# Kernel tuning notes

Hardware: AMD Instinct MI355X
Metric: run time of the kernel (lower is better)

The kernel has to match this reference:

```python
import jax, jax.numpy as jnp
import numpy as np

N = 50000          # nodes
E = 1_600_000      # edges (avg degree 32)
F_IN = 48          # node features (df columns 1:-1)
H, C = 8, 8        # conv1: 8 heads x 8 channels
NC = 2             # num_classes
NEG_SLOPE = 0.2    # PyG GATConv default leaky_relu slope


def setup_inputs() -> dict:
    key = jax.random.key(0)
    ks = jax.random.split(key, 9)
    s = 0.1
    return {
        "x": jax.random.normal(ks[0], (N, F_IN), jnp.float32),
        "edge_index": jax.random.randint(ks[1], (2, E), 0, N, dtype=jnp.int64),
        "W1": jax.random.normal(ks[2], (F_IN, H * C), jnp.float32) * s,
        "att_src1": jax.random.normal(ks[3], (H, C), jnp.float32) * s,
        "att_dst1": jax.random.normal(ks[4], (H, C), jnp.float32) * s,
        "b1": jnp.zeros((H * C,), jnp.float32),
        "W2": jax.random.normal(ks[5], (H * C, NC), jnp.float32) * s,
        "att_src2": jax.random.normal(ks[6], (1, NC), jnp.float32) * s,
        "att_dst2": jax.random.normal(ks[7], (1, NC), jnp.float32) * s,
        "b2": jnp.zeros((NC,), jnp.float32),
    }


def _gat_conv(x, src, dst, W, a_src, a_dst, b, heads, out_ch, concat):
    """PyG GATConv: linear -> per-edge leaky_relu attention -> segment softmax
    over destination nodes -> scatter-sum aggregation."""
    n = x.shape[0]
    h = (x @ W).reshape(n, heads, out_ch)               # [N, H, C]
    e_src = (h * a_src).sum(-1)                          # [N, H]
    e_dst = (h * a_dst).sum(-1)                          # [N, H]
    e = jax.nn.leaky_relu(e_src[src] + e_dst[dst], NEG_SLOPE)  # [E, H]
    # numerically stable segment softmax over incoming edges of each dst node
    m = jax.ops.segment_max(e, dst, num_segments=n)      # [N, H]
    ex = jnp.exp(e - m[dst])
    den = jax.ops.segment_sum(ex, dst, num_segments=n)   # [N, H]
    alpha = ex / den[dst]                                # [E, H]
    out = jax.ops.segment_sum(h[src] * alpha[:, :, None], dst, num_segments=n)
    out = out.reshape(n, heads * out_ch) if concat else out.mean(axis=1)
    return out + b


def reference(x, edge_index, W1, att_src1, att_dst1, b1, W2, att_src2, att_dst2, b2):
    n = x.shape[0]
    loop = jnp.arange(n, dtype=edge_index.dtype)  # GATConv add_self_loops=True
    src = jnp.concatenate([edge_index[0], loop])
    dst = jnp.concatenate([edge_index[1], loop])
    h = _gat_conv(x, src, dst, W1, att_src1, att_dst1, b1, H, C, True)
    h = jax.nn.elu(h)
    out = _gat_conv(h, src, dst, W2, att_src2, att_dst2, b2, 1, NC, False)
    return jax.nn.log_softmax(out, axis=1)
```

## Files before the change

### kernel.cpp

```cpp
#include <hip/hip_runtime.h>
#include <hip/hip_bf16.h>
#include <math.h>

#define NN 50000
#define FIN 48
#define HC 64
#define NHEAD 8
#define NCH 8
#define NCLS 2
#define NEG 0.2f
#define LOG2E 1.44269504f

#define NPB 98
#define NBKT 512
#define CAP 4096
#define BCHUNK 4096


__global__ void k_bin_h1(const int* __restrict__ ei, int* __restrict__ bcur,
                         int* __restrict__ pairs, int e, int tot, int nbin,
                         const float* __restrict__ x, const float* __restrict__ W1,
                         const float* __restrict__ as1, const float* __restrict__ ad1,
                         __hip_bfloat16* __restrict__ h1b, __hip_bfloat16* __restrict__ es1b,
                         float* __restrict__ ed1, int n) {
    __shared__ int hist[NBKT];
    __shared__ int gbase[NBKT];
    __shared__ float Wl[FIN * HC];
    __shared__ float xs[4][FIN];
    __shared__ float hr[4][HC];
    int t = threadIdx.x;
    if ((int)blockIdx.x < nbin) {
        hist[t] = 0; hist[t + 256] = 0;
        __syncthreads();
        int base = blockIdx.x * BCHUNK;
        int end = min(base + BCHUNK, tot);
        int pk[16];
        int bp[16];
        #pragma unroll
        for (int k = 0; k < 16; ++k) {
            int i = base + t + k * 256;
            if (i < end) {
                int s, d;
                if (i < e) { s = ei[i]; d = ei[e + i]; }
                else       { s = d = i - e; }
                int b = d / NPB;
                int p = atomicAdd(&hist[b], 1);
                pk[k] = ((d - b * NPB) << 16) | s;
                bp[k] = (b << 16) | p;
            }
        }
        __syncthreads();
        for (int u = t; u < NBKT; u += 256) {
            int h = hist[u];
            gbase[u] = h ? atomicAdd(&bcur[u], h) : 0;
        }
        __syncthreads();
        #pragma unroll
        for (int k = 0; k < 16; ++k) {
            int i = base + t + k * 256;
            if (i < end) {
                int b = bp[k] >> 16;
                int p = gbase[b] + (bp[k] & 0xFFFF);
                if (p < CAP) pairs[b * CAP + p] = pk[k];
            }
        }
    } else {
        for (int i = t; i < FIN * HC; i += 256) Wl[i] = W1[i];
        int ngroups = (n + 3) >> 2;
        int nl = t >> 6, j = t & 63;
        for (int g = blockIdx.x - nbin; g < ngroups; g += gridDim.x - nbin) {
            int nb = g * 4;
            __syncthreads();
            for (int i = t; i < 4 * FIN; i += 256) {
                int l = i / FIN, k = i % FIN;
                int nd = nb + l;
                xs[l][k] = (nd < n) ? x[nd * FIN + k] : 0.f;
            }
            __syncthreads();
            float acc = 0.f;
            #pragma unroll
            for (int k = 0; k < FIN; ++k) acc += xs[nl][k] * Wl[k * HC + j];
            int nd = nb + nl;
            if (nd < n) h1b[nd * HC + j] = __float2bfloat16(acc);
            hr[nl][j] = acc;
            __syncthreads();
            if (j < 16 && nd < n) {
                int hh = j & 7;
                const float* av = (j < 8) ? as1 : ad1;
                float ev = 0.f;
                #pragma unroll
                for (int c = 0; c < NCH; ++c) ev += hr[nl][hh * NCH + c] * av[hh * NCH + c];
                ev *= LOG2E;
                if (j < 8) es1b[nd * NHEAD + hh] = __float2bfloat16(ev);
                else       ed1[nd * NHEAD + hh] = ev;
            }
        }
    }
}


__global__ void k_bucket_csr(const int* __restrict__ pairs, const int* __restrict__ bcur,
                             int* __restrict__ rowptr, int* __restrict__ degv,
                             int* __restrict__ csr, int n) {
    __shared__ int hist[256];
    int b = blockIdx.x, t = threadIdx.x;
    int lo = b * NPB;
    int nn = min(NPB, n - lo);
    if (nn <= 0) return;
    int base = b * CAP;
    int cnt = min(bcur[b], CAP);
    hist[t] = 0;
    __syncthreads();
    int srcv[16];
    int kp[16];
    #pragma unroll
    for (int k = 0; k < 16; ++k) {
        int i = t + k * 256;
        if (i < cnt) {
            int p = pairs[base + i];
            int key = p >> 16;
            int pos = atomicAdd(&hist[key], 1);
            srcv[k] = p & 0xFFFF;
            kp[k] = (key << 16) | pos;
        }
    }
    __syncthreads();
    int v = hist[t];
    for (int off = 1; off < 256; off <<= 1) {
        int y = (t >= off) ? hist[t - off] : 0;
        __syncthreads();
        hist[t] += y;
        __syncthreads();
    }
    int excl = hist[t] - v;
    if (t < nn) { rowptr[lo + t] = base + excl; degv[lo + t] = v; }
    __syncthreads();
    hist[t] = excl;
    __syncthreads();
    #pragma unroll
    for (int k = 0; k < 16; ++k) {
        int i = t + k * 256;
        if (i < cnt) {
            int key = kp[k] >> 16, pos = kp[k] & 0xFFFF;
            csr[base + hist[key] + pos] = srcv[k];
        }
    }
}


__global__ void k_agg1(const __hip_bfloat16* __restrict__ h1b, const __hip_bfloat16* __restrict__ es1b,
                       const float* __restrict__ ed1, const int* __restrict__ rowptr,
                       const int* __restrict__ degv, const int* __restrict__ csr,
                       const float* __restrict__ b1,
                       const float* __restrict__ W2, const float* __restrict__ as2,
                       const float* __restrict__ ad2, float4* __restrict__ node2, int n) {
    int wid = (blockIdx.x * blockDim.x + threadIdx.x) >> 6;
    if (wid >= n) return;
    int lane = threadIdx.x & 63;
    int j  = lane >> 3;
    int hw = lane & 7;
    int e4 = lane >> 4;
    int r  = lane & 15;
    int ha = r >> 1;
    int ch0 = (ha << 3) + ((r & 1) << 2);
    int wbase = (e4 << 3) + ha;
    int start = rowptr[wid];
    int cnt = degv[wid];
    float edv = ed1[wid * NHEAD + hw];
    float sumw = 0.f;
    float a0 = 0.f, a1 = 0.f, a2 = 0.f, a3 = 0.f;
    int nbatch = cnt >> 3;

    int rv = csr[start + min(lane, cnt - 1)];

    int sl; float ev; uint2 va, vb;
    if (nbatch > 0) {
        sl = __shfl(rv, j, 64);
        ev = __bfloat162float(es1b[sl * NHEAD + hw]);
        int su0 = __shfl(sl, e4 << 3, 64);
        int su1 = __shfl(sl, (4 + e4) << 3, 64);
        va = *(const uint2*)(h1b + su0 * HC + ch0);
        vb = *(const uint2*)(h1b + su1 * HC + ch0);
        for (int b = 1; b < nbatch; ++b) {
            int sl_n;
            if (b < 8) sl_n = __shfl(rv, (b << 3) + j, 64);
            else       sl_n = csr[start + (b << 3) + j];
            float ev_n = __bfloat162float(es1b[sl_n * NHEAD + hw]);
            int su0n = __shfl(sl_n, e4 << 3, 64);
            int su1n = __shfl(sl_n, (4 + e4) << 3, 64);
            uint2 va_n = *(const uint2*)(h1b + su0n * HC + ch0);
            uint2 vb_n = *(const uint2*)(h1b + su1n * HC + ch0);
            float tt = ev + edv;
            tt = fmaxf(tt, NEG * tt);
            float w = exp2f(tt);
            sumw += w;
            float wj0 = __shfl(w, wbase, 64);
            float wj1 = __shfl(w, wbase + 32, 64);
            a0 += wj0 * __uint_as_float(va.x << 16);
            a1 += wj0 * __uint_as_float(va.x & 0xffff0000u);
            a2 += wj0 * __uint_as_float(va.y << 16);
            a3 += wj0 * __uint_as_float(va.y & 0xffff0000u);
            a0 += wj1 * __uint_as_float(vb.x << 16);
            a1 += wj1 * __uint_as_float(vb.x & 0xffff0000u);
            a2 += wj1 * __uint_as_float(vb.y << 16);
            a3 += wj1 * __uint_as_float(vb.y & 0xffff0000u);
            sl = sl_n; ev = ev_n; va = va_n; vb = vb_n;
        }
        float tt = ev + edv;
        tt = fmaxf(tt, NEG * tt);
        float w = exp2f(tt);
        sumw += w;
        float wj0 = __shfl(w, wbase, 64);
        float wj1 = __shfl(w, wbase + 32, 64);
        a0 += wj0 * __uint_as_float(va.x << 16);
        a1 += wj0 * __uint_as_float(va.x & 0xffff0000u);
        a2 += wj0 * __uint_as_float(va.y << 16);
        a3 += wj0 * __uint_as_float(va.y & 0xffff0000u);
        a0 += wj1 * __uint_as_float(vb.x << 16);
        a1 += wj1 * __uint_as_float(vb.x & 0xffff0000u);
        a2 += wj1 * __uint_as_float(vb.y << 16);
        a3 += wj1 * __uint_as_float(vb.y & 0xffff0000u);
    }
    int i = nbatch << 3;
    if (i < cnt) {
        int idx = min(i + j, cnt - 1);
        int slt = (cnt <= 64) ? __shfl(rv, idx, 64) : csr[start + idx];
        float evt = __bfloat162float(es1b[slt * NHEAD + hw]) + edv;
        evt = fmaxf(evt, NEG * evt);
        float w = (i + j < cnt) ? exp2f(evt) : 0.f;
        sumw += w;
        #pragma unroll
        for (int it = 0; it < 2; ++it) {
            int su   = __shfl(slt, ((it << 2) + e4) << 3, 64);
            float wj = __shfl(w, wbase + (it << 5), 64);
            uint2 v = *(const uint2*)(h1b + su * HC + ch0);
            a0 += wj * __uint_as_float(v.x << 16);
            a1 += wj * __uint_as_float(v.x & 0xffff0000u);
            a2 += wj * __uint_as_float(v.y << 16);
            a3 += wj * __uint_as_float(v.y & 0xffff0000u);
        }
    }
    sumw += __shfl_xor(sumw, 8, 64);
    sumw += __shfl_xor(sumw, 16, 64);
    sumw += __shfl_xor(sumw, 32, 64);
    a0 += __shfl_xor(a0, 16, 64); a0 += __shfl_xor(a0, 32, 64);
    a1 += __shfl_xor(a1, 16, 64); a1 += __shfl_xor(a1, 32, 64);
    a2 += __shfl_xor(a2, 16, 64); a2 += __shfl_xor(a2, 32, 64);
    a3 += __shfl_xor(a3, 16, 64); a3 += __shfl_xor(a3, 32, 64);
    float sden = __shfl(sumw, ha, 64);
    float4 bv = *(const float4*)(b1 + ch0);
    float o0 = a0 / sden + bv.x;
    float o1 = a1 / sden + bv.y;
    float o2 = a2 / sden + bv.z;
    float o3 = a3 / sden + bv.w;
    o0 = o0 > 0.f ? o0 : expm1f(o0);
    o1 = o1 > 0.f ? o1 : expm1f(o1);
    o2 = o2 > 0.f ? o2 : expm1f(o2);
    o3 = o3 > 0.f ? o3 : expm1f(o3);
    float4 w01 = *(const float4*)(W2 + ch0 * 2);
    float4 w23 = *(const float4*)(W2 + ch0 * 2 + 4);
    float p0 = o0 * w01.x + o1 * w01.z + o2 * w23.x + o3 * w23.z;
    float p1 = o0 * w01.y + o1 * w01.w + o2 * w23.y + o3 * w23.w;
    #pragma unroll
    for (int off = 8; off > 0; off >>= 1) {
        p0 += __shfl_xor(p0, off, 64);
        p1 += __shfl_xor(p1, off, 64);
    }
    if (lane == 0) {
        float es2v = (p0 * as2[0] + p1 * as2[1]) * LOG2E;
        float ed2v = (p0 * ad2[0] + p1 * ad2[1]) * LOG2E;
        node2[wid] = make_float4(es2v, p0, p1, ed2v);
    }
}


__global__ void k_agg2(const float4* __restrict__ node2, const int* __restrict__ rowptr,
                       const int* __restrict__ degv, const int* __restrict__ csr,
                       const float* __restrict__ b2, float* __restrict__ out, int n) {
    int lane = threadIdx.x & 63;
    int wid = ((blockIdx.x * blockDim.x + threadIdx.x) >> 6) * 4 + (lane >> 4);
    if (wid >= n) return;
    int l16 = lane & 15;
    int start = rowptr[wid];
    int cnt = degv[wid];
    float edv = ((const float*)node2)[wid * 4 + 3];
    float sw = 0.f, a0 = 0.f, a1 = 0.f;
    for (int i = l16; i < cnt; i += 16) {
        int s = __builtin_nontemporal_load(csr + start + i);
        float4 t = node2[s];
        float val = t.x + edv;
        val = fmaxf(val, NEG * val);
        float w = exp2f(val);
        sw += w;
        a0 += w * t.y;
        a1 += w * t.z;
    }
    #pragma unroll
    for (int off = 8; off > 0; off >>= 1) {
        sw += __shfl_xor(sw, off, 16);
        a0 += __shfl_xor(a0, off, 16);
        a1 += __shfl_xor(a1, off, 16);
    }
    if (l16 == 0) {
        float z0 = a0 / sw + b2[0];
        float z1 = a1 / sw + b2[1];
        float mz = fmaxf(z0, z1);
        float lse = mz + logf(__expf(z0 - mz) + __expf(z1 - mz));
        out[wid * NCLS + 0] = z0 - lse;
        out[wid * NCLS + 1] = z1 - lse;
    }
}


extern "C" void kernel_launch(void* const* d_in, const int* in_sizes, int n_in,
                              void* d_out, int out_size, void* d_ws, size_t ws_size,
                              hipStream_t stream) {
    const float* x   = (const float*)d_in[0];
    const int*   ei  = (const int*)d_in[1];
    const float* W1  = (const float*)d_in[2];
    const float* as1 = (const float*)d_in[3];
    const float* ad1 = (const float*)d_in[4];
    const float* b1  = (const float*)d_in[5];
    const float* W2  = (const float*)d_in[6];
    const float* as2 = (const float*)d_in[7];
    const float* ad2 = (const float*)d_in[8];
    const float* b2  = (const float*)d_in[9];
    float* out = (float*)d_out;

    const int n = in_sizes[0] / FIN;
    const int e = in_sizes[1] / 2;
    const int tot = e + n;

    char* ws = (char*)d_ws;
    size_t off = 0;
    auto alloc = [&](size_t bytes) -> void* {
        void* p = ws + off;
        off += (bytes + 255) & ~(size_t)255;
        return p;
    };
    __hip_bfloat16* h1b  = (__hip_bfloat16*)alloc((size_t)n * HC * 2);
    __hip_bfloat16* es1b = (__hip_bfloat16*)alloc((size_t)n * NHEAD * 2);
    int* pairs   = (int*)alloc((size_t)NBKT * CAP * 4);
    int* csr     = (int*)alloc((size_t)NBKT * CAP * 4);
    float* ed1   = (float*)alloc((size_t)n * NHEAD * 4);
    float4* node2 = (float4*)alloc((size_t)n * 16);
    int* rowptr  = (int*)alloc((size_t)n * 4);
    int* degv    = (int*)alloc((size_t)n * 4);
    int* bcur    = (int*)alloc(NBKT * 4);

    const int nbin = (tot + BCHUNK - 1) / BCHUNK;

    hipMemsetAsync(bcur, 0, NBKT * 4, stream);
    k_bin_h1<<<nbin + 1024, 256, 0, stream>>>(ei, bcur, pairs, e, tot, nbin,
                                              x, W1, as1, ad1, h1b, es1b, ed1, n);
    k_bucket_csr<<<NBKT, 256, 0, stream>>>(pairs, bcur, rowptr, degv, csr, n);
    k_agg1<<<(n * 64 + 255) / 256, 256, 0, stream>>>(h1b, es1b, ed1, rowptr, degv, csr,
                                                     b1, W2, as2, ad2, node2, n);
    k_agg2<<<(n * 16 + 255) / 256, 256, 0, stream>>>(node2, rowptr, degv, csr, b2, out, n);
}
```

Before: 111.0 us.

## Stage binned pairs in LDS for coalesced writes and double-buffer the h1 GEMM

The binning blocks now take half-size chunks and sort each chunk's pairs by bucket in shared memory, using a block prefix scan. The pairs are then written out contiguously, so global stores are coalesced instead of scattered. The h1 projection path processes 8 nodes per iteration with double-buffered x tiles. It computes the attention logits with wavefront shuffles instead of a shared-memory reduction pass. The memset is replaced by a small zero kernel. The costs are an extra scan with many barriers, a larger shared-memory union, and more binning blocks.

```diff
diff --git a/kernel.cpp b/kernel.cpp
--- a/kernel.cpp
+++ b/kernel.cpp
@@ -14,7 +14,12 @@
 #define NPB 98
 #define NBKT 512
 #define CAP 4096
-#define BCHUNK 4096
+#define BCHUNK 2048
+
+__global__ void k_zero(int* p, int n) {
+    int i = blockIdx.x * blockDim.x + threadIdx.x;
+    if (i < n) p[i] = 0;
+}
 
 
 __global__ void k_bin_h1(const int* __restrict__ ei, int* __restrict__ bcur,
@@ -23,77 +28,116 @@
                          const float* __restrict__ as1, const float* __restrict__ ad1,
                          __hip_bfloat16* __restrict__ h1b, __hip_bfloat16* __restrict__ es1b,
                          float* __restrict__ ed1, int n) {
-    __shared__ int hist[NBKT];
-    __shared__ int gbase[NBKT];
-    __shared__ float Wl[FIN * HC];
-    __shared__ float xs[4][FIN];
-    __shared__ float hr[4][HC];
+    __shared__ union SM {
+        struct { int hist[NBKT]; int gbase[NBKT]; int pay[BCHUNK]; int dst[BCHUNK]; } bin;
+        struct { float Wl[FIN * HC]; float xs[2][8][FIN]; } g;
+    } sm;
     int t = threadIdx.x;
     if ((int)blockIdx.x < nbin) {
-        hist[t] = 0; hist[t + 256] = 0;
+        sm.bin.hist[t] = 0; sm.bin.hist[t + 256] = 0;
         __syncthreads();
         int base = blockIdx.x * BCHUNK;
         int end = min(base + BCHUNK, tot);
-        int pk[16];
-        int bp[16];
+        int cntb = end - base;
+        int pk[8];
+        int bp[8];
         #pragma unroll
-        for (int k = 0; k < 16; ++k) {
+        for (int k = 0; k < 8; ++k) {
             int i = base + t + k * 256;
             if (i < end) {
                 int s, d;
                 if (i < e) { s = ei[i]; d = ei[e + i]; }
                 else       { s = d = i - e; }
                 int b = d / NPB;
-                int p = atomicAdd(&hist[b], 1);
+                int p = atomicAdd(&sm.bin.hist[b], 1);
                 pk[k] = ((d - b * NPB) << 16) | s;
                 bp[k] = (b << 16) | p;
             }
         }
         __syncthreads();
-        for (int u = t; u < NBKT; u += 256) {
-            int h = hist[u];
-            gbase[u] = h ? atomicAdd(&bcur[u], h) : 0;
-        }
+        int c0 = sm.bin.hist[2 * t], c1 = sm.bin.hist[2 * t + 1];
+        sm.bin.gbase[2 * t]     = c0 ? atomicAdd(&bcur[2 * t], c0) : 0;
+        sm.bin.gbase[2 * t + 1] = c1 ? atomicAdd(&bcur[2 * t + 1], c1) : 0;
+        int s = c0 + c1;
+        sm.bin.dst[t] = s;
+        __syncthreads();
+        for (int off = 1; off < 256; off <<= 1) {
+            int y = (t >= off) ? sm.bin.dst[t - off] : 0;
+            __syncthreads();
+            sm.bin.dst[t] += y;
+            __syncthreads();
+        }
+        int excl = sm.bin.dst[t] - s;
+        sm.bin.hist[2 * t] = excl;
+        sm.bin.hist[2 * t + 1] = excl + c0;
         __syncthreads();
         #pragma unroll
-        for (int k = 0; k < 16; ++k) {
+        for (int k = 0; k < 8; ++k) {
             int i = base + t + k * 256;
             if (i < end) {
-                int b = bp[k] >> 16;
-                int p = gbase[b] + (bp[k] & 0xFFFF);
-                if (p < CAP) pairs[b * CAP + p] = pk[k];
+                int b = bp[k] >> 16, pos = bp[k] & 0xFFFF;
+                int q = sm.bin.hist[b] + pos;
+                int off2 = sm.bin.gbase[b] + pos;
+                sm.bin.pay[q] = pk[k];
+                sm.bin.dst[q] = (off2 < CAP) ? (b * CAP + off2) : -1;
             }
         }
+        __syncthreads();
+        for (int q = t; q < cntb; q += 256) {
+            int dq = sm.bin.dst[q];
+            if (dq >= 0) pairs[dq] = sm.bin.pay[q];
+        }
     } else {
-        for (int i = t; i < FIN * HC; i += 256) Wl[i] = W1[i];
-        int ngroups = (n + 3) >> 2;
-        int nl = t >> 6, j = t & 63;
-        for (int g = blockIdx.x - nbin; g < ngroups; g += gridDim.x - nbin) {
-            int nb = g * 4;
-            __syncthreads();
-            for (int i = t; i < 4 * FIN; i += 256) {
+        for (int i = t; i < FIN * HC; i += 256) sm.g.Wl[i] = W1[i];
+        int j = t & 63, nl = t >> 6;
+        float asl = as1[j] * LOG2E, adl = ad1[j] * LOG2E;
+        int hh = j >> 3, c = j & 7;
+        int GB = gridDim.x - nbin;
+        int ngroups = (n + 7) >> 3;
+        int g = blockIdx.x - nbin;
+        if (g < ngroups) {
+            int nb = g * 8;
+            for (int i = t; i < 8 * FIN; i += 256) {
                 int l = i / FIN, k = i % FIN;
                 int nd = nb + l;
-                xs[l][k] = (nd < n) ? x[nd * FIN + k] : 0.f;
+                sm.g.xs[0][l][k] = (nd < n) ? x[nd * FIN + k] : 0.f;
             }
+        }
+        __syncthreads();
+        int cur = 0;
+        for (; g < ngroups; ) {
+            int gn = g + GB;
+            if (gn < ngroups) {
+                int nb = gn * 8;
+                for (int i = t; i < 8 * FIN; i += 256) {
+                    int l = i / FIN, k = i % FIN;
+                    int nd = nb + l;
+                    sm.g.xs[cur ^ 1][l][k] = (nd < n) ? x[nd * FIN + k] : 0.f;
+                }
+            }
+            int nb = g * 8;
+            float acc0 = 0.f, acc1 = 0.f;
+            #pragma unroll
+            for (int k = 0; k < FIN; ++k) {
+                float wv = sm.g.Wl[k * HC + j];
+                acc0 += sm.g.xs[cur][nl][k] * wv;
+                acc1 += sm.g.xs[cur][nl + 4][k] * wv;
+            }
+            int nd0 = nb + nl, nd1 = nb + nl + 4;
+            if (nd0 < n) h1b[nd0 * HC + j] = __float2bfloat16(acc0);
+            if (nd1 < n) h1b[nd1 * HC + j] = __float2bfloat16(acc1);
+            float e0s = acc0 * asl, e0d = acc0 * adl;
+            float e1s = acc1 * asl, e1d = acc1 * adl;
+            e0s += __shfl_xor(e0s, 1, 64); e0s += __shfl_xor(e0s, 2, 64); e0s += __shfl_xor(e0s, 4, 64);
+            e0d += __shfl_xor(e0d, 1, 64); e0d += __shfl_xor(e0d, 2, 64); e0d += __shfl_xor(e0d, 4, 64);
+            e1s += __shfl_xor(e1s, 1, 64); e1s += __shfl_xor(e1s, 2, 64); e1s += __shfl_xor(e1s, 4, 64);
+            e1d += __shfl_xor(e1d, 1, 64); e1d += __shfl_xor(e1d, 2, 64); e1d += __shfl_xor(e1d, 4, 64);
+            if (c == 0 && nd0 < n) es1b[nd0 * NHEAD + hh] = __float2bfloat16(e0s);
+            if (c == 1 && nd0 < n) ed1[nd0 * NHEAD + hh] = e0d;
+            if (c == 0 && nd1 < n) es1b[nd1 * NHEAD + hh] = __float2bfloat16(e1s);
+            if (c == 1 && nd1 < n) ed1[nd1 * NHEAD + hh] = e1d;
             __syncthreads();
-            float acc = 0.f;
-            #pragma unroll
-            for (int k = 0; k < FIN; ++k) acc += xs[nl][k] * Wl[k * HC + j];
-            int nd = nb + nl;
-            if (nd < n) h1b[nd * HC + j] = __float2bfloat16(acc);
-            hr[nl][j] = acc;
-            __syncthreads();
-            if (j < 16 && nd < n) {
-                int hh = j & 7;
-                const float* av = (j < 8) ? as1 : ad1;
-                float ev = 0.f;
-                #pragma unroll
-                for (int c = 0; c < NCH; ++c) ev += hr[nl][hh * NCH + c] * av[hh * NCH + c];
-                ev *= LOG2E;
-                if (j < 8) es1b[nd * NHEAD + hh] = __float2bfloat16(ev);
-                else       ed1[nd * NHEAD + hh] = ev;
-            }
+            cur ^= 1; g = gn;
         }
     }
 }
@@ -350,7 +394,7 @@
 
     const int nbin = (tot + BCHUNK - 1) / BCHUNK;
 
-    hipMemsetAsync(bcur, 0, NBKT * 4, stream);
+    k_zero<<<(NBKT + 255) / 256, 256, 0, stream>>>(bcur, NBKT);
     k_bin_h1<<<nbin + 1024, 256, 0, stream>>>(ei, bcur, pairs, e, tot, nbin,
                                               x, W1, as1, ad1, h1b, es1b, ed1, n);
     k_bucket_csr<<<NBKT, 256, 0, stream>>>(pairs, bcur, rowptr, degv, csr, n);
```

Result: slower. 132.2 us (+19.1%).
